# Kernel optimization log

Measured on AMD Instinct MI355X. Metric: run time of the kernel, lower is better.

## Reference

```python
import jax, jax.numpy as jnp
import numpy as np
import math

D_MODEL = 1024
N_HEAD = 16
HEAD_DIM = D_MODEL // N_HEAD
BATCH = 4
MAX_LEN = 1024


def _shift(BD):
    # BD: (b, h, L, 2L) -> (b, h, L, L), Transformer-XL relative shift
    b, h, L, _ = BD.shape
    zero_pad = jnp.zeros((b, h, L, 1), BD.dtype)
    BD = jnp.concatenate([BD, zero_pad], axis=-1)      # (b,h,L,2L+1)
    BD = BD.reshape(b, h, -1, L)[:, :, :-1]            # (b,h,2L,L)
    BD = BD.reshape(b, h, L, -1)                       # (b,h,L,2L)
    return BD[:, :, :, L:]                             # (b,h,L,L)


def setup_inputs() -> dict:
    key = jax.random.key(0)
    ks = jax.random.split(key, 10)
    s = 1.0 / math.sqrt(D_MODEL)
    return {
        "q": jax.random.normal(ks[0], (BATCH, MAX_LEN, D_MODEL), jnp.float32),
        "k": jax.random.normal(ks[1], (BATCH, MAX_LEN, D_MODEL), jnp.float32),
        "mask": jax.random.randint(ks[2], (BATCH, MAX_LEN), 0, 2, jnp.int32),
        "pos_embed": jax.random.normal(ks[3], (2 * MAX_LEN, HEAD_DIM), jnp.float32),
        "Wq": jax.random.normal(ks[4], (D_MODEL, D_MODEL), jnp.float32) * s,
        "Wkv": jax.random.normal(ks[5], (D_MODEL, 2 * D_MODEL), jnp.float32) * s,
        "Wr": jax.random.normal(ks[6], (HEAD_DIM, HEAD_DIM), jnp.float32) / math.sqrt(HEAD_DIM),
        "r_r_bias": jax.random.normal(ks[7], (N_HEAD, HEAD_DIM), jnp.float32) * 0.02,
        "r_w_bias": jax.random.normal(ks[8], (N_HEAD, HEAD_DIM), jnp.float32) * 0.02,
    }


def reference(q, k, mask, pos_embed, Wq, Wkv, Wr, r_r_bias, r_w_bias):
    B, L, D = q.shape
    H = r_r_bias.shape[0]
    hd = D // H
    scale = math.sqrt(hd)

    r = pos_embed @ Wr                                   # (2L, hd)
    qh = (q @ Wq).reshape(B, L, H, hd).transpose(0, 2, 1, 3)   # (B,H,L,hd)
    kv = k @ Wkv                                         # (B,L,2D)
    kk, vv = jnp.split(kv, 2, axis=-1)
    kh = kk.reshape(B, L, H, hd).transpose(0, 2, 1, 3)
    vh = vv.reshape(B, L, H, hd).transpose(0, 2, 1, 3)

    AC = jnp.einsum('bhqd,bhkd->bhqk', qh + r_r_bias[None, :, None, :], kh)
    BD = jnp.einsum('bhqd,ld->bhql', qh + r_w_bias[None, :, None, :], r)  # (B,H,L,2L)
    BD = _shift(BD)

    attn = (AC + BD) / scale
    attn = jnp.where(mask[:, None, None, :] == 0, -jnp.inf, attn)
    attn = jax.nn.softmax(attn, axis=-1)

    out = jnp.einsum('bhqk,bhkd->bhqd', attn, vh)        # (B,H,L,hd)
    return out.transpose(0, 2, 1, 3).reshape(B, L, D)
```

## Files before the change

### kernel.cpp

```cpp
#include <hip/hip_runtime.h>

typedef short bf16x8 __attribute__((ext_vector_type(8)));
typedef float f32x4 __attribute__((ext_vector_type(4)));
typedef unsigned short u16;
typedef unsigned short u16x4 __attribute__((ext_vector_type(4)));
typedef unsigned short u16x8 __attribute__((ext_vector_type(8)));
typedef unsigned int u32;

#define NB 4
#define LEN 1024
#define DM 1024
#define NH 16
#define HD 64

#define QSCALE 0.18033688011112043f

__device__ __forceinline__ u16 f2bf(float f) {
    union { float f; unsigned u; } v; v.f = f;
    return (u16)((v.u + 0x7fffu + ((v.u >> 16) & 1u)) >> 16);
}

__device__ __forceinline__ float exp2f_fast(float x) {
    float r; asm("v_exp_f32 %0, %1" : "=v"(r) : "v"(x)); return r;
}

__device__ __forceinline__ unsigned cvt_pk_bf16(float a, float b) {
    unsigned r; asm("v_cvt_pk_bf16_f32 %0, %1, %2" : "=v"(r) : "v"(a), "v"(b)); return r;
}

__device__ __forceinline__ f32x4 mfma16(bf16x8 a, bf16x8 b, f32x4 c) {
    return __builtin_amdgcn_mfma_f32_16x16x32_bf16(a, b, c, 0, 0, 0);
}

__device__ __forceinline__ void gload16(const void* g, void* l) {
    __builtin_amdgcn_global_load_lds(
        (const __attribute__((address_space(1))) unsigned int*)g,
        (__attribute__((address_space(3))) unsigned int*)l, 16, 0, 0);
}

__global__ void prep(const float* __restrict__ q, const float* __restrict__ k,
                     const int* __restrict__ msk,
                     const float* __restrict__ Wq, const float* __restrict__ Wkv,
                     const float* __restrict__ pos, const float* __restrict__ Wr,
                     u16* __restrict__ qbf, u16* __restrict__ kbf,
                     u16* __restrict__ WqT, u16* __restrict__ WkvT,
                     u16* __restrict__ rbf, float* __restrict__ mb) {
    __shared__ float tile[32][33];
    const int f = blockIdx.x;
    const int tid = threadIdx.x;
    if (f < 3072) {
        const int x = f % 96, y = f / 96;
        const bool isQ = x < 32;
        const float* W = isQ ? Wq : Wkv;
        u16* WT = isQ ? WqT : WkvT;
        const int N = isQ ? 1024 : 2048;
        const int n0 = (isQ ? x : x - 32) * 32;
        const int k0 = y * 32;
        const int tx = tid & 31, ty = tid >> 5;
        #pragma unroll
        for (int j = 0; j < 4; j++) {
            int r = ty + j * 8;
            tile[r][tx] = W[(size_t)(k0 + r) * N + n0 + tx];
        }
        __syncthreads();
        #pragma unroll
        for (int j = 0; j < 4; j++) {
            int r = ty + j * 8;
            WT[(size_t)(n0 + r) * 1024 + k0 + tx] = f2bf(tile[tx][r]);
        }
    } else if (f < 3588) {
        int idx = (f - 3072) * 256 + tid;
        if (idx < 2064 * 64) {
            int row = idx >> 6, col = idx & 63;
            float s = 0.f;
            if (row < 2048) {
                #pragma unroll
                for (int kk = 0; kk < 64; kk++) s += pos[row * 64 + kk] * Wr[kk * 64 + col];
            }
            const int csw = (((col >> 3) ^ (row & 7)) << 3) | (col & 7);
            rbf[(row << 6) | csw] = f2bf(s);
        }
    } else if (f < 3604) {
        int i = (f - 3588) * 256 + tid;
        if (i < NB * LEN) mb[i] = msk[i] ? 0.f : -3.0e38f;
    } else {
        int idx = (f - 3604) * 256 + tid;
        if (idx < 1048576) {
            float4 v = ((const float4*)q)[idx];
            u16x4 o;
            o[0] = f2bf(v.x); o[1] = f2bf(v.y); o[2] = f2bf(v.z); o[3] = f2bf(v.w);
            ((u16x4*)qbf)[idx] = o;
        } else if (idx < 2097152) {
            int i = idx - 1048576;
            float4 v = ((const float4*)k)[i];
            u16x4 o;
            o[0] = f2bf(v.x); o[1] = f2bf(v.y); o[2] = f2bf(v.z); o[3] = f2bf(v.w);
            ((u16x4*)kbf)[i] = o;
        }
    }
}

__global__ __launch_bounds__(256) void gemm_all(
    const u16* __restrict__ qbf, const u16* __restrict__ kbf,
    const u16* __restrict__ WqT, const u16* __restrict__ WkvT,
    const float* __restrict__ rrb, const float* __restrict__ rwb,
    u16* __restrict__ A1, u16* __restrict__ A2,
    u16* __restrict__ khs, u16* __restrict__ vhsT)
{
    __shared__ u16 as[2][128][32];
    __shared__ u16 bs[2][128][32];

    const int fb = blockIdx.x;
    const int wsw = ((fb & 7) * 96) + (fb >> 3);
    const int bx = wsw % 24;
    const bool isQ = bx < 8;
    const u16* Abf = isQ ? qbf : kbf;
    const u16* BT  = isQ ? WqT : WkvT;
    const int n0 = (isQ ? bx : bx - 8) * 128;
    const int m0 = (wsw / 24) * 128;
    const int tid = threadIdx.x;
    const int w = tid >> 6, lane = tid & 63, g = lane >> 4, c = lane & 15;
    const int wm = w >> 1, wn = w & 1;
    const int srow = lane >> 2, sj = lane & 3;

    const f32x4 fzero = {0.f, 0.f, 0.f, 0.f};
    f32x4 acc[4][4];
    #pragma unroll
    for (int i = 0; i < 4; i++)
        #pragma unroll
        for (int j = 0; j < 4; j++) acc[i][j] = fzero;

    auto STAGE = [&](int buf, int ks) {
        const int k0 = ks * 32;
        #pragma unroll
        for (int i = 0; i < 2; i++) {
            const int rb = w * 32 + i * 16;
            const int rowA = rb + srow;
            gload16(Abf + (size_t)(m0 + rowA) * 1024 + k0 + ((sj ^ (rowA & 3)) << 3),
                    &as[buf][rb][0]);
            gload16(BT + (size_t)(n0 + rowA) * 1024 + k0 + ((sj ^ (rowA & 3)) << 3),
                    &bs[buf][rb][0]);
        }
    };

    STAGE(0, 0);
    __syncthreads();

    for (int ks = 0; ks < 32; ks++) {
        const int cur = ks & 1, nb = cur ^ 1;
        if (ks < 31) STAGE(nb, ks + 1);

        bf16x8 af[4], bfr[4];
        #pragma unroll
        for (int i = 0; i < 4; i++) {
            const int row = wm * 64 + i * 16 + c;
            af[i] = *(const bf16x8*)&as[cur][row][(g ^ (row & 3)) << 3];
        }
        #pragma unroll
        for (int j = 0; j < 4; j++) {
            const int row = wn * 64 + j * 16 + c;
            bfr[j] = *(const bf16x8*)&bs[cur][row][(g ^ (row & 3)) << 3];
        }
        #pragma unroll
        for (int i = 0; i < 4; i++)
            #pragma unroll
            for (int j = 0; j < 4; j++)
                acc[i][j] = mfma16(af[i], bfr[j], acc[i][j]);

        __syncthreads();
    }

    #pragma unroll
    for (int j = 0; j < 4; j++) {
        const int n = n0 + wn * 64 + j * 16 + c;
        float b1v = 0.f, b2v = 0.f;
        if (isQ) { b1v = rrb[n]; b2v = rwb[n]; }
        #pragma unroll
        for (int i = 0; i < 4; i++) {
            const int l0 = m0 + wm * 64 + i * 16 + 4 * g;
            if (!isQ && n >= DM) {
                const int d = n & 63, hh = (n - DM) >> 6;
                const int bb = l0 >> 10, l = l0 & 1023;
                u16x4 o;
                #pragma unroll
                for (int r = 0; r < 4; r++) o[r] = f2bf(acc[i][j][r]);
                *(u16x4*)(vhsT + (((size_t)(bb * NH + hh)) * HD + d) * LEN + l) = o;
            } else {
                #pragma unroll
                for (int r = 0; r < 4; r++) {
                    const int row = l0 + r;
                    const int bb = row >> 10, l = row & 1023;
                    const float v = acc[i][j][r];
                    if (isQ) {
                        size_t idx = (((size_t)(bb * NH + (n >> 6))) * LEN + l) * HD + (n & 63);
                        A1[idx] = f2bf((v + b1v) * QSCALE);
                        A2[idx] = f2bf((v + b2v) * QSCALE);
                    } else {
                        const int d = n & 63;
                        const int dsw = (((d >> 3) ^ (l & 7)) << 3) | (d & 7);
                        size_t idx = (((size_t)(bb * NH + (n >> 6))) * LEN + l) * HD + dsw;
                        khs[idx] = f2bf(v);
                    }
                }
            }
        }
    }
}

__global__ __launch_bounds__(512, 4) void attn_kernel(
    const u16* __restrict__ A1, const u16* __restrict__ A2,
    const u16* __restrict__ khs, const u16* __restrict__ vhsT,
    const u16* __restrict__ rbf, const float* __restrict__ mbias,
    float* __restrict__ outp)
{
    __shared__ u16 kbuf[2][32][64];
    __shared__ u16 rbuf[192][64];
    __shared__ u16 vbuf[2][4][64][8];
    __shared__ float biasl[1024];
    __shared__ float gl[8][16][52];
    __shared__ u16 pl[8][16][40];

    const int bh = blockIdx.x;
    const int b = bh >> 4, h = bh & 15;
    const int tid = threadIdx.x;
    const int w = tid >> 6, lane = tid & 63, g = lane >> 4, c = lane & 15;
    const int q0 = blockIdx.y * 128, q0w = q0 + w * 16;
    const int lrow8 = lane >> 3, lcol = lane & 7;
    const int kkey = (c + 1) & 7;

    const u16* Kbase = khs + (size_t)bh * LEN * HD;
    const u16* Vp = vhsT + (size_t)bh * HD * LEN;
    u16* plw = &pl[w][0][0];
    float* glw = &gl[w][0][0];

    const u16* A1p = A1 + ((size_t)bh * LEN + q0w) * HD;
    const u16* A2p = A2 + ((size_t)bh * LEN + q0w) * HD;
    bf16x8 a1f[2], a2f[2];
    #pragma unroll
    for (int kf = 0; kf < 2; kf++) {
        a1f[kf] = *(const bf16x8*)(A1p + c * HD + kf * 32 + g * 8);
        a2f[kf] = *(const bf16x8*)(A2p + c * HD + kf * 32 + g * 8);
    }

    const int js0 = LEN - q0 - 128;
    if (w < 4) {
        gload16(Kbase + (((size_t)(8 * w + lrow8)) << 6) + (lcol << 3), &kbuf[0][8 * w][0]);
        gload16(Vp + ((size_t)lane << 10) + 8 * w, &vbuf[0][w][0][0]);
        const int gr = 16 + w;
        gload16(rbf + (((size_t)(js0 + 8 * gr + lrow8)) << 6) + (lcol << 3), &rbuf[(js0 + 8 * gr) % 192][0]);
    } else {
        gload16(mbias + b * LEN + (w - 4) * 256 + lane * 4, &biasl[(w - 4) * 256]);
    }
    #pragma unroll
    for (int i = 0; i < 2; i++) {
        const int gr = w + 8 * i;
        gload16(rbf + (((size_t)(js0 + 8 * gr + lrow8)) << 6) + (lcol << 3), &rbuf[(js0 + 8 * gr) % 192][0]);
    }
    __syncthreads();

    const f32x4 fzero = {0.f, 0.f, 0.f, 0.f};
    f32x4 oacc[4];
    #pragma unroll
    for (int dt = 0; dt < 4; dt++) oacc[dt] = fzero;
    float mrow = -3.0e38f, lrow = 0.f;

    for (int kt = 0; kt < 32; kt++) {
        const int cur = kt & 1, nb = cur ^ 1;
        const int c0 = kt * 32;

        if (kt < 31) {
            const int c0n = c0 + 32;
            if (w < 4) {
                gload16(Kbase + (((size_t)(c0n + 8 * w + lrow8)) << 6) + (lcol << 3), &kbuf[nb][8 * w][0]);
                gload16(Vp + ((size_t)lane << 10) + c0n + 8 * w, &vbuf[nb][w][0][0]);
            } else {
                const int row0 = js0 + 160 + 32 * kt + 8 * (w - 4);
                gload16(rbf + (((size_t)(row0 + lrow8)) << 6) + (lcol << 3), &rbuf[row0 % 192][0]);
            }
        }

        bf16x8 Kf[2][2];
        #pragma unroll
        for (int ct = 0; ct < 2; ct++)
            #pragma unroll
            for (int kf = 0; kf < 2; kf++)
                Kf[ct][kf] = *(const bf16x8*)&kbuf[cur][16 * ct + c][((4 * kf + g) ^ (c & 7)) * 8];

        const int bs = (1009 - q0w + 32 * kt) % 192;
        bf16x8 Rf[3][2];
        #pragma unroll
        for (int mt = 0; mt < 3; mt++) {
            int t = bs + mt * 16 + c; if (t >= 192) t -= 192;
            #pragma unroll
            for (int kf = 0; kf < 2; kf++)
                Rf[mt][kf] = *(const bf16x8*)&rbuf[t][((4 * kf + g) ^ kkey) * 8];
        }

        __builtin_amdgcn_s_setprio(1);
        f32x4 s0 = fzero, s1 = fzero;
        s0 = mfma16(Kf[0][0], a1f[0], s0);
        s0 = mfma16(Kf[0][1], a1f[1], s0);
        s1 = mfma16(Kf[1][0], a1f[0], s1);
        s1 = mfma16(Kf[1][1], a1f[1], s1);
        f32x4 g0 = fzero, g1 = fzero, g2 = fzero;
        g0 = mfma16(Rf[0][0], a2f[0], g0);
        g0 = mfma16(Rf[0][1], a2f[1], g0);
        *(f32x4*)&glw[c * 52 + 4 * g] = g0;
        g1 = mfma16(Rf[1][0], a2f[0], g1);
        g1 = mfma16(Rf[1][1], a2f[1], g1);
        *(f32x4*)&glw[c * 52 + 16 + 4 * g] = g1;
        g2 = mfma16(Rf[2][0], a2f[0], g2);
        g2 = mfma16(Rf[2][1], a2f[1], g2);
        *(f32x4*)&glw[c * 52 + 32 + 4 * g] = g2;
        __builtin_amdgcn_s_setprio(0);

        const float* glq = &glw[c * 52];
        f32x4 bb0 = *(const f32x4*)&biasl[c0 + 4 * g];
        f32x4 bb1 = *(const f32x4*)&biasl[c0 + 16 + 4 * g];
        #pragma unroll
        for (int r = 0; r < 4; r++) {
            const int gidx = 4 * g + r + 15 - c;
            s0[r] += glq[gidx] + bb0[r];
            s1[r] += glq[gidx + 16] + bb1[r];
        }

        float t = fmaxf(fmaxf(fmaxf(s0[0], s0[1]), fmaxf(s0[2], s0[3])),
                        fmaxf(fmaxf(s1[0], s1[1]), fmaxf(s1[2], s1[3])));
        t = fmaxf(t, __shfl_xor(t, 16));
        t = fmaxf(t, __shfl_xor(t, 32));
        if (!__all(t <= mrow + 8.f)) {
            const float mnew = fmaxf(mrow, t);
            const float alpha = exp2f_fast(mrow - mnew);
            mrow = mnew;
            lrow *= alpha;
            #pragma unroll
            for (int dt = 0; dt < 4; dt++)
                #pragma unroll
                for (int r = 0; r < 4; r++) oacc[dt][r] *= alpha;
        }
        float p[8];
        float ps = 0.f;
        #pragma unroll
        for (int r = 0; r < 4; r++) {
            p[r] = exp2f_fast(s0[r] - mrow);
            p[4 + r] = exp2f_fast(s1[r] - mrow);
            ps += p[r] + p[4 + r];
        }
        lrow += ps;
        const unsigned d0 = cvt_pk_bf16(p[0], p[1]);
        const unsigned d1 = cvt_pk_bf16(p[2], p[3]);
        const unsigned d2 = cvt_pk_bf16(p[4], p[5]);
        const unsigned d3 = cvt_pk_bf16(p[6], p[7]);
        const int prow = c * 40;
        *(uint2*)&plw[prow + 4 * g] = make_uint2(d0, d1);
        *(uint2*)&plw[prow + 16 + 4 * g] = make_uint2(d2, d3);
        bf16x8 pbr = *(const bf16x8*)&plw[prow + 8 * g];

        bf16x8 Vb[4];
        #pragma unroll
        for (int dt = 0; dt < 4; dt++)
            Vb[dt] = *(const bf16x8*)&vbuf[cur][g][16 * dt + c][0];
        __builtin_amdgcn_s_setprio(1);
        #pragma unroll
        for (int dt = 0; dt < 4; dt++)
            oacc[dt] = mfma16(Vb[dt], pbr, oacc[dt]);
        __builtin_amdgcn_s_setprio(0);

        __syncthreads();
    }

    float sum = lrow;
    sum += __shfl_xor(sum, 16);
    sum += __shfl_xor(sum, 32);
    const float inv = sum > 0.f ? 1.0f / sum : 0.f;
    const int l = q0w + c;
    float* op = outp + ((size_t)b * LEN + l) * DM + h * HD;
    #pragma unroll
    for (int dt = 0; dt < 4; dt++) {
        f32x4 o;
        #pragma unroll
        for (int r = 0; r < 4; r++) o[r] = oacc[dt][r] * inv;
        *(f32x4*)(op + dt * 16 + 4 * g) = o;
    }
}

extern "C" void kernel_launch(void* const* d_in, const int* in_sizes, int n_in,
                              void* d_out, int out_size, void* d_ws, size_t ws_size,
                              hipStream_t stream) {
    const float* q   = (const float*)d_in[0];
    const float* k   = (const float*)d_in[1];
    const int*   msk = (const int*)d_in[2];
    const float* pos = (const float*)d_in[3];
    const float* Wq  = (const float*)d_in[4];
    const float* Wkv = (const float*)d_in[5];
    const float* Wr  = (const float*)d_in[6];
    const float* rrb = (const float*)d_in[7];
    const float* rwb = (const float*)d_in[8];
    float* outp = (float*)d_out;
    char* ws = (char*)d_ws;

    u16* qbf  = (u16*)(ws + 0);
    u16* kbf  = (u16*)(ws + 8388608);
    u16* WqT  = (u16*)(ws + 16777216);
    u16* WkvT = (u16*)(ws + 18874368);
    u16* rbf  = (u16*)(ws + 23068672);
    u16* A1   = (u16*)(ws + 23332864);
    u16* A2   = (u16*)(ws + 31721472);
    u16* khs  = (u16*)(ws + 40110080);
    u16* vhsT = (u16*)(ws + 48498688);
    float* mb = (float*)(ws + 56887296);

    prep<<<11796, 256, 0, stream>>>(q, k, msk, Wq, Wkv, pos, Wr, qbf, kbf, WqT, WkvT, rbf, mb);
    gemm_all<<<768, 256, 0, stream>>>(qbf, kbf, WqT, WkvT, rrb, rwb, A1, A2, khs, vhsT);
    attn_kernel<<<dim3(64, 8), 512, 0, stream>>>(A1, A2, khs, vhsT, rbf, mb, outp);
}
```

Baseline: 117.1 us.

## Derive A2 in-kernel from A1, reuse R fragments across steps, alias P buffer

The GEMM no longer writes the second scaled query tensor (A2). The attention kernel rebuilds it from A1 plus the difference of the two bias vectors, which removes an 8 MB write and its re-read. The attention loop is unrolled by two so the last relative-position fragment of one step becomes the first of the next, cutting one of three LDS fragment loads per step; the R ring buffer grows from 192 to 224 rows to match. The P staging buffer now aliases the per-warp score-gather scratch to save LDS. Rebuilding A2 from an already bf16-rounded A1 adds a second rounding, so A2 may differ slightly from before.

```diff
diff --git a/kernel.cpp b/kernel.cpp
--- a/kernel.cpp
+++ b/kernel.cpp
@@ -18,6 +18,11 @@
 __device__ __forceinline__ u16 f2bf(float f) {
     union { float f; unsigned u; } v; v.f = f;
     return (u16)((v.u + 0x7fffu + ((v.u >> 16) & 1u)) >> 16);
+}
+
+__device__ __forceinline__ float bf2f(u16 x) {
+    union { float f; unsigned u; } v; v.u = ((unsigned)x) << 16;
+    return v.f;
 }
 
 __device__ __forceinline__ float exp2f_fast(float x) {
@@ -103,8 +108,8 @@
 __global__ __launch_bounds__(256) void gemm_all(
     const u16* __restrict__ qbf, const u16* __restrict__ kbf,
     const u16* __restrict__ WqT, const u16* __restrict__ WkvT,
-    const float* __restrict__ rrb, const float* __restrict__ rwb,
-    u16* __restrict__ A1, u16* __restrict__ A2,
+    const float* __restrict__ rrb,
+    u16* __restrict__ A1,
     u16* __restrict__ khs, u16* __restrict__ vhsT)
 {
     __shared__ u16 as[2][128][32];
@@ -173,8 +178,8 @@
     #pragma unroll
     for (int j = 0; j < 4; j++) {
         const int n = n0 + wn * 64 + j * 16 + c;
-        float b1v = 0.f, b2v = 0.f;
-        if (isQ) { b1v = rrb[n]; b2v = rwb[n]; }
+        float b1v = 0.f;
+        if (isQ) b1v = rrb[n];
         #pragma unroll
         for (int i = 0; i < 4; i++) {
             const int l0 = m0 + wm * 64 + i * 16 + 4 * g;
@@ -194,7 +199,6 @@
                     if (isQ) {
                         size_t idx = (((size_t)(bb * NH + (n >> 6))) * LEN + l) * HD + (n & 63);
                         A1[idx] = f2bf((v + b1v) * QSCALE);
-                        A2[idx] = f2bf((v + b2v) * QSCALE);
                     } else {
                         const int d = n & 63;
                         const int dsw = (((d >> 3) ^ (l & 7)) << 3) | (d & 7);
@@ -208,17 +212,17 @@
 }
 
 __global__ __launch_bounds__(512, 4) void attn_kernel(
-    const u16* __restrict__ A1, const u16* __restrict__ A2,
+    const u16* __restrict__ A1,
     const u16* __restrict__ khs, const u16* __restrict__ vhsT,
     const u16* __restrict__ rbf, const float* __restrict__ mbias,
+    const float* __restrict__ rrb, const float* __restrict__ rwb,
     float* __restrict__ outp)
 {
     __shared__ u16 kbuf[2][32][64];
-    __shared__ u16 rbuf[192][64];
+    __shared__ u16 rbuf[224][64];
     __shared__ u16 vbuf[2][4][64][8];
     __shared__ float biasl[1024];
     __shared__ float gl[8][16][52];
-    __shared__ u16 pl[8][16][40];
 
     const int bh = blockIdx.x;
     const int b = bh >> 4, h = bh & 15;
@@ -230,33 +234,61 @@
 
     const u16* Kbase = khs + (size_t)bh * LEN * HD;
     const u16* Vp = vhsT + (size_t)bh * HD * LEN;
-    u16* plw = &pl[w][0][0];
     float* glw = &gl[w][0][0];
+    u16* pw = (u16*)glw;
 
     const u16* A1p = A1 + ((size_t)bh * LEN + q0w) * HD;
-    const u16* A2p = A2 + ((size_t)bh * LEN + q0w) * HD;
     bf16x8 a1f[2], a2f[2];
     #pragma unroll
-    for (int kf = 0; kf < 2; kf++) {
+    for (int kf = 0; kf < 2; kf++)
         a1f[kf] = *(const bf16x8*)(A1p + c * HD + kf * 32 + g * 8);
-        a2f[kf] = *(const bf16x8*)(A2p + c * HD + kf * 32 + g * 8);
+    {
+        const float* rrbp = rrb + h * HD;
+        const float* rwbp = rwb + h * HD;
+        #pragma unroll
+        for (int kf = 0; kf < 2; kf++) {
+            const int dbase = kf * 32 + g * 8;
+            f32x4 rA0 = *(const f32x4*)(rrbp + dbase);
+            f32x4 rA1 = *(const f32x4*)(rrbp + dbase + 4);
+            f32x4 rB0 = *(const f32x4*)(rwbp + dbase);
+            f32x4 rB1 = *(const f32x4*)(rwbp + dbase + 4);
+            float a2v[8];
+            #pragma unroll
+            for (int e = 0; e < 4; e++) {
+                a2v[e]     = bf2f((u16)a1f[kf][e])     + (rB0[e] - rA0[e]) * QSCALE;
+                a2v[4 + e] = bf2f((u16)a1f[kf][4 + e]) + (rB1[e] - rA1[e]) * QSCALE;
+            }
+            union { u32 u[4]; bf16x8 v; } cv;
+            cv.u[0] = cvt_pk_bf16(a2v[0], a2v[1]);
+            cv.u[1] = cvt_pk_bf16(a2v[2], a2v[3]);
+            cv.u[2] = cvt_pk_bf16(a2v[4], a2v[5]);
+            cv.u[3] = cvt_pk_bf16(a2v[6], a2v[7]);
+            a2f[kf] = cv.v;
+        }
     }
 
     const int js0 = LEN - q0 - 128;
     if (w < 4) {
         gload16(Kbase + (((size_t)(8 * w + lrow8)) << 6) + (lcol << 3), &kbuf[0][8 * w][0]);
         gload16(Vp + ((size_t)lane << 10) + 8 * w, &vbuf[0][w][0][0]);
-        const int gr = 16 + w;
-        gload16(rbf + (((size_t)(js0 + 8 * gr + lrow8)) << 6) + (lcol << 3), &rbuf[(js0 + 8 * gr) % 192][0]);
     } else {
         gload16(mbias + b * LEN + (w - 4) * 256 + lane * 4, &biasl[(w - 4) * 256]);
     }
     #pragma unroll
-    for (int i = 0; i < 2; i++) {
-        const int gr = w + 8 * i;
-        gload16(rbf + (((size_t)(js0 + 8 * gr + lrow8)) << 6) + (lcol << 3), &rbuf[(js0 + 8 * gr) % 192][0]);
+    for (int i = 0; i < 3; i++) {
+        const int row = js0 + 8 * (w + 8 * i);
+        gload16(rbf + (((size_t)(row + lrow8)) << 6) + (lcol << 3), &rbuf[row % 224][0]);
     }
     __syncthreads();
+
+    bf16x8 RA[2], RB[2];
+    int bs = (1009 - q0w) % 224;
+    {
+        int t = bs + c; if (t >= 224) t -= 224;
+        #pragma unroll
+        for (int kf = 0; kf < 2; kf++)
+            RA[kf] = *(const bf16x8*)&rbuf[t][((4 * kf + g) ^ kkey) * 8];
+    }
 
     const f32x4 fzero = {0.f, 0.f, 0.f, 0.f};
     f32x4 oacc[4];
@@ -264,18 +296,20 @@
     for (int dt = 0; dt < 4; dt++) oacc[dt] = fzero;
     float mrow = -3.0e38f, lrow = 0.f;
 
-    for (int kt = 0; kt < 32; kt++) {
+    auto STEP = [&](int kt, bf16x8 (&Rold)[2], bf16x8 (&Rnew)[2]) {
         const int cur = kt & 1, nb = cur ^ 1;
         const int c0 = kt * 32;
 
-        if (kt < 31) {
-            const int c0n = c0 + 32;
-            if (w < 4) {
+        if (w < 4) {
+            if (kt < 31) {
+                const int c0n = c0 + 32;
                 gload16(Kbase + (((size_t)(c0n + 8 * w + lrow8)) << 6) + (lcol << 3), &kbuf[nb][8 * w][0]);
                 gload16(Vp + ((size_t)lane << 10) + c0n + 8 * w, &vbuf[nb][w][0][0]);
-            } else {
-                const int row0 = js0 + 160 + 32 * kt + 8 * (w - 4);
-                gload16(rbf + (((size_t)(row0 + lrow8)) << 6) + (lcol << 3), &rbuf[row0 % 192][0]);
+            }
+        } else {
+            if (kt < 30) {
+                const int row0 = js0 + 192 + 32 * kt + 8 * (w - 4);
+                gload16(rbf + (((size_t)(row0 + lrow8)) << 6) + (lcol << 3), &rbuf[row0 % 224][0]);
             }
         }
 
@@ -286,14 +320,20 @@
             for (int kf = 0; kf < 2; kf++)
                 Kf[ct][kf] = *(const bf16x8*)&kbuf[cur][16 * ct + c][((4 * kf + g) ^ (c & 7)) * 8];
 
-        const int bs = (1009 - q0w + 32 * kt) % 192;
-        bf16x8 Rf[3][2];
-        #pragma unroll
-        for (int mt = 0; mt < 3; mt++) {
-            int t = bs + mt * 16 + c; if (t >= 192) t -= 192;
+        bf16x8 Rf1[2], Rf2[2];
+        {
+            int t = bs + 16 + c; if (t >= 224) t -= 224;
             #pragma unroll
             for (int kf = 0; kf < 2; kf++)
-                Rf[mt][kf] = *(const bf16x8*)&rbuf[t][((4 * kf + g) ^ kkey) * 8];
+                Rf1[kf] = *(const bf16x8*)&rbuf[t][((4 * kf + g) ^ kkey) * 8];
+        }
+        {
+            int t = bs + 32 + c; if (t >= 224) t -= 224;
+            #pragma unroll
+            for (int kf = 0; kf < 2; kf++) {
+                Rf2[kf] = *(const bf16x8*)&rbuf[t][((4 * kf + g) ^ kkey) * 8];
+                Rnew[kf] = Rf2[kf];
+            }
         }
 
         __builtin_amdgcn_s_setprio(1);
@@ -303,14 +343,14 @@
         s1 = mfma16(Kf[1][0], a1f[0], s1);
         s1 = mfma16(Kf[1][1], a1f[1], s1);
         f32x4 g0 = fzero, g1 = fzero, g2 = fzero;
-        g0 = mfma16(Rf[0][0], a2f[0], g0);
-        g0 = mfma16(Rf[0][1], a2f[1], g0);
+        g0 = mfma16(Rold[0], a2f[0], g0);
+        g0 = mfma16(Rold[1], a2f[1], g0);
         *(f32x4*)&glw[c * 52 + 4 * g] = g0;
-        g1 = mfma16(Rf[1][0], a2f[0], g1);
-        g1 = mfma16(Rf[1][1], a2f[1], g1);
+        g1 = mfma16(Rf1[0], a2f[0], g1);
+        g1 = mfma16(Rf1[1], a2f[1], g1);
         *(f32x4*)&glw[c * 52 + 16 + 4 * g] = g1;
-        g2 = mfma16(Rf[2][0], a2f[0], g2);
-        g2 = mfma16(Rf[2][1], a2f[1], g2);
+        g2 = mfma16(Rf2[0], a2f[0], g2);
+        g2 = mfma16(Rf2[1], a2f[1], g2);
         *(f32x4*)&glw[c * 52 + 32 + 4 * g] = g2;
         __builtin_amdgcn_s_setprio(0);
 
@@ -351,10 +391,9 @@
         const unsigned d1 = cvt_pk_bf16(p[2], p[3]);
         const unsigned d2 = cvt_pk_bf16(p[4], p[5]);
         const unsigned d3 = cvt_pk_bf16(p[6], p[7]);
-        const int prow = c * 40;
-        *(uint2*)&plw[prow + 4 * g] = make_uint2(d0, d1);
-        *(uint2*)&plw[prow + 16 + 4 * g] = make_uint2(d2, d3);
-        bf16x8 pbr = *(const bf16x8*)&plw[prow + 8 * g];
+        *(uint2*)&pw[c * 104 + 4 * g] = make_uint2(d0, d1);
+        *(uint2*)&pw[c * 104 + 16 + 4 * g] = make_uint2(d2, d3);
+        bf16x8 pbr = *(const bf16x8*)&pw[c * 104 + 8 * g];
 
         bf16x8 Vb[4];
         #pragma unroll
@@ -366,7 +405,13 @@
             oacc[dt] = mfma16(Vb[dt], pbr, oacc[dt]);
         __builtin_amdgcn_s_setprio(0);
 
+        bs += 32; if (bs >= 224) bs -= 224;
         __syncthreads();
+    };
+
+    for (int kt2 = 0; kt2 < 16; kt2++) {
+        STEP(2 * kt2,     RA, RB);
+        STEP(2 * kt2 + 1, RB, RA);
     }
 
     float sum = lrow;
@@ -405,12 +450,11 @@
     u16* WkvT = (u16*)(ws + 18874368);
     u16* rbf  = (u16*)(ws + 23068672);
     u16* A1   = (u16*)(ws + 23332864);
-    u16* A2   = (u16*)(ws + 31721472);
     u16* khs  = (u16*)(ws + 40110080);
     u16* vhsT = (u16*)(ws + 48498688);
     float* mb = (float*)(ws + 56887296);
 
     prep<<<11796, 256, 0, stream>>>(q, k, msk, Wq, Wkv, pos, Wr, qbf, kbf, WqT, WkvT, rbf, mb);
-    gemm_all<<<768, 256, 0, stream>>>(qbf, kbf, WqT, WkvT, rrb, rwb, A1, A2, khs, vhsT);
-    attn_kernel<<<dim3(64, 8), 512, 0, stream>>>(A1, A2, khs, vhsT, rbf, mb, outp);
-}
+    gemm_all<<<768, 256, 0, stream>>>(qbf, kbf, WqT, WkvT, rrb, A1, khs, vhsT);
+    attn_kernel<<<dim3(64, 8), 512, 0, stream>>>(A1, khs, vhsT, rbf, mb, rrb, rwb, outp);
+}
```

Result: faster. 113.6 us, median of 2 (-2.9%).
